# Kernel optimization log

Hardware: AMD Instinct MI355X
Metric: run time of the kernel (lower is better)

## Reference

```python
import math
import jax, jax.numpy as jnp
import numpy as np

D_MODEL = 2048
NUM_EXPERTS = 64
Z_LOSS_COEF = 1e-3
AUX_LOSS_COEF = 1e-2
CAPACITY_FACTOR = 1.0
MIN_CAPACITY = 4


def setup_inputs() -> dict:
    key = jax.random.key(0)
    kx, kw = jax.random.split(key)
    x = jax.random.normal(kx, (4, 4096, D_MODEL), dtype=jnp.float32)
    W = 0.02 * jax.random.normal(kw, (NUM_EXPERTS, D_MODEL), dtype=jnp.float32)  # gate weight [E, D]
    return {"x": x, "W": W}


def reference(x, W):
    B, T, D = x.shape
    N = B * T                      # num_tokens
    E = W.shape[0]
    x_flat = x.reshape(N, D)

    logits = jnp.einsum("nd,ed->ne", x_flat, W)          # gate GEMM [N, E]
    probs = jax.nn.softmax(logits, axis=-1)

    # z-loss: mean(logsumexp(logits)^2)
    z_loss = jnp.mean(jnp.square(jax.nn.logsumexp(logits, axis=-1)))

    expert_index = jnp.argmax(logits, axis=-1)            # [N] int
    expert_prob = jnp.take_along_axis(probs, expert_index[:, None], axis=-1)[:, 0]  # [N]

    counts = jnp.bincount(expert_index, length=E)         # [E] int
    f_i = counts.astype(probs.dtype) / N                  # fraction routed per expert
    p_i = jnp.mean(probs, axis=0)                         # mean router prob per expert
    aux_loss = AUX_LOSS_COEF * E * jnp.sum(f_i * p_i) + Z_LOSS_COEF * z_loss

    capacity = max(MIN_CAPACITY, math.ceil(CAPACITY_FACTOR * N / E))  # static int
    return expert_index, expert_prob, counts, capacity, aux_loss
```

## Files before the change

kernel.cpp:

```cpp
#include <hip/hip_runtime.h>
#include <math.h>

#define D_MODEL 2048
#define NE      64
#define TB      64
#define KHALF   1024
#define KC      64
#define NCH     (KHALF / KC)
#define FB_KC   32
#define FB_NCH  (D_MODEL / FB_KC)

typedef _Float16 half8 __attribute__((ext_vector_type(8)));
typedef float    f32x4 __attribute__((ext_vector_type(4)));

#define CVT1(F, HV, LV, J) do {                                               \
    float _f = (F);                                                           \
    _Float16 _h = (_Float16)_f;                                               \
    HV[J] = _h;                                                               \
    LV[J] = (_Float16)(_f - (float)_h);                                       \
} while (0)

__global__ __launch_bounds__(256) void wcvt_kernel(
    const float* __restrict__ W, short* __restrict__ Wh, short* __restrict__ Wl)
{
    const int e = blockIdx.x, t = threadIdx.x, c = t * 8;
    const float* src = W + (size_t)e * D_MODEL + c;
    float4 v0 = *(const float4*)src;
    float4 v1 = *(const float4*)(src + 4);
    half8 hv, lv;
    CVT1(v0.x * 64.0f, hv, lv, 0); CVT1(v0.y * 64.0f, hv, lv, 1);
    CVT1(v0.z * 64.0f, hv, lv, 2); CVT1(v0.w * 64.0f, hv, lv, 3);
    CVT1(v1.x * 64.0f, hv, lv, 4); CVT1(v1.y * 64.0f, hv, lv, 5);
    CVT1(v1.z * 64.0f, hv, lv, 6); CVT1(v1.w * 64.0f, hv, lv, 7);
    *(half8*)(Wh + (size_t)e * D_MODEL + c) = hv;
    *(half8*)(Wl + (size_t)e * D_MODEL + c) = lv;
}

__global__ __launch_bounds__(512, 2) void router_fused_v3(
    const float* __restrict__ x, const short* __restrict__ Whg,
    const short* __restrict__ Wlg, float* __restrict__ out,
    float* __restrict__ ws_prob, float* __restrict__ ws_z,
    int* __restrict__ ws_cnt, int Ntok)
{
    __shared__ __align__(16) char smem[65536];

    const int t  = threadIdx.x;
    const int b  = blockIdx.x;
    const int m0 = b * TB;
    const int g  = t >> 8;
    const int tg = t & 255;
    const int l  = tg & 63;
    const int wv = tg >> 6;
    const int k0 = g * KHALF;

    char* gbase = smem + g * 32768;

    float (*sL)[NE + 1] = (float (*)[NE + 1])smem;
    float (*red8)[8]    = (float (*)[8])(smem + 16640);
    int   (*arg8)[8]    = (int (*)[8])(smem + 18688);
    float* smax         = (float*)(smem + 20736);
    float* sinv         = (float*)(smem + 20992);
    float (*spart)[NE]  = (float (*)[NE])(smem + 21248);
    int*   hist         = (int*)(smem + 23296);

    const int srow = tg >> 2;
    const int sc   = tg & 3;
    const int ssw  = srow & 7;
    const int sof0 = (srow << 6) + (((sc * 2 + 0) ^ ssw) << 3);
    const int sof1 = (srow << 6) + (((sc * 2 + 1) ^ ssw) << 3);
    const size_t wsrc = (size_t)srow * D_MODEL + k0 + sc * 16;

    const float* abase = x + (size_t)(m0 + wv * 16 + (l & 15)) * D_MODEL
                           + k0 + ((l >> 4) * 8);

    f32x4 acc0 = {0.f,0.f,0.f,0.f}, acc1 = {0.f,0.f,0.f,0.f};
    f32x4 acc2 = {0.f,0.f,0.f,0.f}, acc3 = {0.f,0.f,0.f,0.f};

    uint4  whA0, whA1, wlA0, wlA1;
    uint4  whB0, whB1, wlB0, wlB1;
    float4 aA0, aA1, aA2, aA3;
    float4 aB0, aB1, aB2, aB3;

#define PRE_W(WH0, WH1, WL0, WL1, CH) do {                                    \
    const size_t _o = wsrc + (size_t)(CH) * KC;                               \
    WH0 = *(const uint4*)&Whg[_o];     WH1 = *(const uint4*)&Whg[_o + 8];     \
    WL0 = *(const uint4*)&Wlg[_o];     WL1 = *(const uint4*)&Wlg[_o + 8];     \
} while (0)

#define STORE_W(WH0, WH1, WL0, WL1, BB) do {                                  \
    _Float16* _Wh = (_Float16*)(gbase + (BB) * 16384);                        \
    _Float16* _Wl = (_Float16*)(gbase + (BB) * 16384 + 8192);                 \
    *(uint4*)&_Wh[sof0] = WH0;  *(uint4*)&_Wh[sof1] = WH1;                    \
    *(uint4*)&_Wl[sof0] = WL0;  *(uint4*)&_Wl[sof1] = WL1;                    \
} while (0)

#define PRE_A(PA0, PA1, PA2, PA3, CH) do {                                    \
    const float* _a0 = abase + (size_t)(CH) * KC;                             \
    const float* _a1 = _a0 + 32;                                              \
    PA0 = *(const float4*)_a0; PA1 = *(const float4*)(_a0 + 4);               \
    PA2 = *(const float4*)_a1; PA3 = *(const float4*)(_a1 + 4);               \
} while (0)

#define MFMA_PHASE(BB, PA0, PA1, PA2, PA3) do {                               \
    const _Float16* _Wh = (const _Float16*)(gbase + (BB) * 16384);            \
    const _Float16* _Wl = (const _Float16*)(gbase + (BB) * 16384 + 8192);     \
    const int _rsw = l & 7;                                                   \
    _Pragma("unroll")                                                         \
    for (int kq = 0; kq < 2; ++kq) {                                          \
        half8 _ah, _al;                                                       \
        if (kq == 0) {                                                        \
            CVT1((PA0).x * 8.0f, _ah, _al, 0); CVT1((PA0).y * 8.0f, _ah, _al, 1); \
            CVT1((PA0).z * 8.0f, _ah, _al, 2); CVT1((PA0).w * 8.0f, _ah, _al, 3); \
            CVT1((PA1).x * 8.0f, _ah, _al, 4); CVT1((PA1).y * 8.0f, _ah, _al, 5); \
            CVT1((PA1).z * 8.0f, _ah, _al, 6); CVT1((PA1).w * 8.0f, _ah, _al, 7); \
        } else {                                                              \
            CVT1((PA2).x * 8.0f, _ah, _al, 0); CVT1((PA2).y * 8.0f, _ah, _al, 1); \
            CVT1((PA2).z * 8.0f, _ah, _al, 2); CVT1((PA2).w * 8.0f, _ah, _al, 3); \
            CVT1((PA3).x * 8.0f, _ah, _al, 4); CVT1((PA3).y * 8.0f, _ah, _al, 5); \
            CVT1((PA3).z * 8.0f, _ah, _al, 6); CVT1((PA3).w * 8.0f, _ah, _al, 7); \
        }                                                                     \
        const int _s = kq * 4 + (l >> 4);                                     \
        _Pragma("unroll")                                                     \
        for (int n = 0; n < 4; ++n) {                                         \
            const int _row  = n * 16 + (l & 15);                              \
            const int _woff = (_row << 6) + (((_s ^ (_row & 7))) << 3);       \
            half8 _wh = *(const half8*)&_Wh[_woff];                           \
            half8 _wl = *(const half8*)&_Wl[_woff];                           \
            f32x4 _a = (n == 0) ? acc0 : (n == 1) ? acc1 : (n == 2) ? acc2 : acc3; \
            _a = __builtin_amdgcn_mfma_f32_16x16x32_f16(_al, _wl, _a, 0, 0, 0); \
            _a = __builtin_amdgcn_mfma_f32_16x16x32_f16(_al, _wh, _a, 0, 0, 0); \
            _a = __builtin_amdgcn_mfma_f32_16x16x32_f16(_ah, _wl, _a, 0, 0, 0); \
            _a = __builtin_amdgcn_mfma_f32_16x16x32_f16(_ah, _wh, _a, 0, 0, 0); \
            if (n == 0) acc0 = _a; else if (n == 1) acc1 = _a;                \
            else if (n == 2) acc2 = _a; else acc3 = _a;                       \
        }                                                                     \
    }                                                                         \
} while (0)

    PRE_W(whA0, whA1, wlA0, wlA1, 0);
    STORE_W(whA0, whA1, wlA0, wlA1, 0);
    PRE_W(whB0, whB1, wlB0, wlB1, 1);
    PRE_A(aA0, aA1, aA2, aA3, 0);
    PRE_A(aB0, aB1, aB2, aB3, 1);
    asm volatile("s_waitcnt lgkmcnt(0)" ::: "memory");
    __builtin_amdgcn_s_barrier();

    for (int ch = 0; ch < NCH; ch += 2) {
        if (ch + 1 < NCH) STORE_W(whB0, whB1, wlB0, wlB1, 1);
        if (ch + 2 < NCH) PRE_W(whA0, whA1, wlA0, wlA1, ch + 2);
        MFMA_PHASE(0, aA0, aA1, aA2, aA3);
        if (ch + 2 < NCH) PRE_A(aA0, aA1, aA2, aA3, ch + 2);
        asm volatile("s_waitcnt lgkmcnt(0)" ::: "memory");
        __builtin_amdgcn_s_barrier();
        if (ch + 2 < NCH) STORE_W(whA0, whA1, wlA0, wlA1, 0);
        if (ch + 3 < NCH) PRE_W(whB0, whB1, wlB0, wlB1, ch + 3);
        MFMA_PHASE(1, aB0, aB1, aB2, aB3);
        if (ch + 3 < NCH) PRE_A(aB0, aB1, aB2, aB3, ch + 3);
        asm volatile("s_waitcnt lgkmcnt(0)" ::: "memory");
        __builtin_amdgcn_s_barrier();
    }

    __syncthreads();
    const int rbase = wv * 16 + (l >> 4) * 4;
    const int col0  = l & 15;
    if (g == 1) {
        #pragma unroll
        for (int q = 0; q < 4; ++q) {
            sL[rbase + q][ 0 + col0] = acc0[q];
            sL[rbase + q][16 + col0] = acc1[q];
            sL[rbase + q][32 + col0] = acc2[q];
            sL[rbase + q][48 + col0] = acc3[q];
        }
    }
    __syncthreads();
    if (g == 0) {
        #pragma unroll
        for (int q = 0; q < 4; ++q) {
            sL[rbase + q][ 0 + col0] = (acc0[q] + sL[rbase + q][ 0 + col0]) * (1.0f / 512.0f);
            sL[rbase + q][16 + col0] = (acc1[q] + sL[rbase + q][16 + col0]) * (1.0f / 512.0f);
            sL[rbase + q][32 + col0] = (acc2[q] + sL[rbase + q][32 + col0]) * (1.0f / 512.0f);
            sL[rbase + q][48 + col0] = (acc3[q] + sL[rbase + q][48 + col0]) * (1.0f / 512.0f);
        }
    }
    if (t < NE) hist[t] = 0;
    __syncthreads();

    {
        const int m = t >> 3, qr = t & 7;
        float mx = -3.4e38f; int ag = qr * 8;
        #pragma unroll
        for (int k = 0; k < 8; ++k) {
            const int e = qr * 8 + k;
            float v = sL[m][e];
            if (v > mx) { mx = v; ag = e; }
        }
        red8[m][qr] = mx; arg8[m][qr] = ag;
    }
    __syncthreads();
    if (t < 64) {
        const int m = t;
        float mx = red8[m][0]; int ag = arg8[m][0];
        #pragma unroll
        for (int qr = 1; qr < 8; ++qr)
            if (red8[m][qr] > mx) { mx = red8[m][qr]; ag = arg8[m][qr]; }
        smax[m] = mx;
        out[m0 + m] = (float)ag;
        atomicAdd(&hist[ag], 1);
    }
    __syncthreads();
    {
        const int m = t >> 3, qr = t & 7;
        const float mx = smax[m];
        float s = 0.f;
        #pragma unroll
        for (int k = 0; k < 8; ++k) s += expf(sL[m][qr * 8 + k] - mx);
        red8[m][qr] = s;
    }
    __syncthreads();
    if (t < 64) {
        const int m = t;
        float s = 0.f;
        #pragma unroll
        for (int qr = 0; qr < 8; ++qr) s += red8[m][qr];
        float inv = 1.f / s;
        sinv[m] = inv;
        out[Ntok + m0 + m] = inv;
        float lse = smax[m] + logf(s);
        float z = lse * lse;
        #pragma unroll
        for (int off = 32; off > 0; off >>= 1) z += __shfl_down(z, off, 64);
        if (t == 0) ws_z[b] = z;
    }
    __syncthreads();
    {
        const int e = t & 63, gw = t >> 6;
        float pa = 0.f;
        #pragma unroll
        for (int k = 0; k < 8; ++k) {
            const int m = gw * 8 + k;
            pa += expf(sL[m][e] - smax[m]) * sinv[m];
        }
        spart[gw][e] = pa;
    }
    __syncthreads();
    if (t < NE) {
        float ps = 0.f;
        #pragma unroll
        for (int gw = 0; gw < 8; ++gw) ps += spart[gw][t];
        ws_prob[b * NE + t] = ps;
        ws_cnt[b * NE + t]  = hist[t];
    }
}

__global__ __launch_bounds__(256) void router_final2(
    const float* __restrict__ ws_prob, const float* __restrict__ ws_z,
    const int* __restrict__ ws_cnt, float* __restrict__ out,
    int Ntok, int nblocks)
{
    __shared__ float sp[4][NE];
    __shared__ int   sc[4][NE];
    __shared__ float sz[4];

    const int e = threadIdx.x & 63, g = threadIdx.x >> 6;
    const int per = nblocks / 4;
    const int hi  = (g == 3) ? nblocks : (g + 1) * per;

    float ps = 0.f; int c = 0;
    for (int blk = g * per; blk < hi; ++blk) {
        ps += ws_prob[blk * NE + e];
        c  += ws_cnt[blk * NE + e];
    }
    sp[g][e] = ps; sc[g][e] = c;

    float z = 0.f;
    for (int blk = (int)threadIdx.x; blk < nblocks; blk += 256) z += ws_z[blk];
    #pragma unroll
    for (int off = 32; off > 0; off >>= 1) z += __shfl_down(z, off, 64);
    if (e == 0) sz[g] = z;
    __syncthreads();

    if (threadIdx.x < 64) {
        const int ee = threadIdx.x;
        float pst = ((sp[0][ee] + sp[1][ee]) + sp[2][ee]) + sp[3][ee];
        int   ct  = ((sc[0][ee] + sc[1][ee]) + sc[2][ee]) + sc[3][ee];
        out[2 * Ntok + ee] = (float)ct;

        float fN = (float)Ntok;
        float fp = ((float)ct / fN) * (pst / fN);
        #pragma unroll
        for (int off = 32; off > 0; off >>= 1) fp += __shfl_down(fp, off, 64);
        if (ee == 0) {
            float zt = ((sz[0] + sz[1]) + sz[2]) + sz[3];
            int cap = (Ntok + NE - 1) / NE;
            if (cap < 4) cap = 4;
            float aux = 0.01f * (float)NE * fp + 1e-3f * (zt / fN);
            out[2 * Ntok + NE]     = (float)cap;
            out[2 * Ntok + NE + 1] = aux;
        }
    }
}

__global__ __launch_bounds__(256) void router_main_fb(
    const float* __restrict__ x, const float* __restrict__ W,
    float* __restrict__ out, float* __restrict__ ws_prob,
    float* __restrict__ ws_z, int* __restrict__ ws_cnt, int Ntok)
{
    __shared__ __align__(16) float sX[FB_KC][68];
    __shared__ __align__(16) float sW[FB_KC][68];
    __shared__ float sL[64][65];
    __shared__ float smax[64], sinv[64];
    __shared__ float spart[4][NE];
    __shared__ int   hist[NE];

    const int t = threadIdx.x, b = blockIdx.x, m0 = b * 64;
    const int mq = t & 15, nq = t >> 4;
    const int r1 = t >> 3, r2 = r1 + 32, c1 = (t & 7) << 2;
    const float* xp1 = x + (size_t)(m0 + r1) * D_MODEL + c1;
    const float* xp2 = x + (size_t)(m0 + r2) * D_MODEL + c1;
    const float* wp1 = W + (size_t)r1 * D_MODEL + c1;
    const float* wp2 = W + (size_t)r2 * D_MODEL + c1;
    float4 ax1 = *(const float4*)xp1, ax2 = *(const float4*)xp2;
    float4 aw1 = *(const float4*)wp1, aw2 = *(const float4*)wp2;
    float a1[4][4] = {}, a2[4][4] = {};
    for (int ch = 0; ch < FB_NCH; ++ch) {
        __syncthreads();
        sX[c1+0][r1] = ax1.x; sX[c1+1][r1] = ax1.y; sX[c1+2][r1] = ax1.z; sX[c1+3][r1] = ax1.w;
        sX[c1+0][r2] = ax2.x; sX[c1+1][r2] = ax2.y; sX[c1+2][r2] = ax2.z; sX[c1+3][r2] = ax2.w;
        sW[c1+0][r1] = aw1.x; sW[c1+1][r1] = aw1.y; sW[c1+2][r1] = aw1.z; sW[c1+3][r1] = aw1.w;
        sW[c1+0][r2] = aw2.x; sW[c1+1][r2] = aw2.y; sW[c1+2][r2] = aw2.z; sW[c1+3][r2] = aw2.w;
        __syncthreads();
        if (ch + 1 < FB_NCH) {
            xp1 += FB_KC; xp2 += FB_KC; wp1 += FB_KC; wp2 += FB_KC;
            ax1 = *(const float4*)xp1; ax2 = *(const float4*)xp2;
            aw1 = *(const float4*)wp1; aw2 = *(const float4*)wp2;
        }
        #pragma unroll
        for (int k = 0; k < FB_KC; ++k) {
            float4 xa = *(const float4*)&sX[k][mq << 2];
            float4 wb = *(const float4*)&sW[k][nq << 2];
            float (*A)[4] = (k < FB_KC / 2) ? a1 : a2;
            A[0][0] = fmaf(xa.x, wb.x, A[0][0]); A[0][1] = fmaf(xa.x, wb.y, A[0][1]);
            A[0][2] = fmaf(xa.x, wb.z, A[0][2]); A[0][3] = fmaf(xa.x, wb.w, A[0][3]);
            A[1][0] = fmaf(xa.y, wb.x, A[1][0]); A[1][1] = fmaf(xa.y, wb.y, A[1][1]);
            A[1][2] = fmaf(xa.y, wb.z, A[1][2]); A[1][3] = fmaf(xa.y, wb.w, A[1][3]);
            A[2][0] = fmaf(xa.z, wb.x, A[2][0]); A[2][1] = fmaf(xa.z, wb.y, A[2][1]);
            A[2][2] = fmaf(xa.z, wb.z, A[2][2]); A[2][3] = fmaf(xa.z, wb.w, A[2][3]);
            A[3][0] = fmaf(xa.w, wb.x, A[3][0]); A[3][1] = fmaf(xa.w, wb.y, A[3][1]);
            A[3][2] = fmaf(xa.w, wb.z, A[3][2]); A[3][3] = fmaf(xa.w, wb.w, A[3][3]);
        }
    }
    #pragma unroll
    for (int i = 0; i < 4; ++i)
        #pragma unroll
        for (int j = 0; j < 4; ++j)
            sL[(mq << 2) + i][(nq << 2) + j] = a1[i][j] + a2[i][j];
    if (t < NE) hist[t] = 0;
    __syncthreads();
    if (t < 64) {
        const int m = t;
        float mx = sL[m][0]; int arg = 0;
        for (int e = 1; e < NE; ++e) { float v = sL[m][e]; if (v > mx) { mx = v; arg = e; } }
        float s = 0.f;
        for (int e = 0; e < NE; ++e) s += expf(sL[m][e] - mx);
        float inv = 1.f / s;
        out[m0 + m] = (float)arg; out[Ntok + m0 + m] = inv;
        smax[m] = mx; sinv[m] = inv;
        atomicAdd(&hist[arg], 1);
        float lse = mx + logf(s); float z = lse * lse;
        for (int off = 32; off > 0; off >>= 1) z += __shfl_down(z, off, 64);
        if (t == 0) ws_z[b] = z;
    }
    __syncthreads();
    {
        const int e = t & 63, mg = t >> 6;
        float pa = 0.f;
        for (int m = mg * 16; m < mg * 16 + 16; ++m) pa += expf(sL[m][e] - smax[m]) * sinv[m];
        spart[mg][e] = pa;
    }
    __syncthreads();
    if (t < NE) {
        ws_prob[b * NE + t] = spart[0][t] + spart[1][t] + spart[2][t] + spart[3][t];
        ws_cnt[b * NE + t]  = hist[t];
    }
}

extern "C" void kernel_launch(void* const* d_in, const int* in_sizes, int n_in,
                              void* d_out, int out_size, void* d_ws, size_t ws_size,
                              hipStream_t stream)
{
    const float* x = (const float*)d_in[0];
    const float* W = (const float*)d_in[1];
    float* out = (float*)d_out;

    const int Ntok = in_sizes[0] / D_MODEL;
    const int nblk = Ntok / TB;

    const size_t wh_elems = (size_t)NE * D_MODEL;
    const size_t need = wh_elems * 2 * 2
                      + ((size_t)nblk * NE + nblk) * 4
                      + (size_t)nblk * NE * 4 + 1024;

    if ((Ntok % TB) == 0 && (nblk % 4) == 0 && ws_size >= need) {
        short* wsh     = (short*)d_ws;
        short* wsl     = wsh + wh_elems;
        float* ws_prob = (float*)(wsl + wh_elems);
        float* ws_z    = ws_prob + (size_t)nblk * NE;
        int*   ws_cnt  = (int*)(ws_z + nblk);

        wcvt_kernel<<<NE, 256, 0, stream>>>(W, wsh, wsl);
        router_fused_v3<<<nblk, 512, 0, stream>>>(x, wsh, wsl, out,
                                                  ws_prob, ws_z, ws_cnt, Ntok);
        router_final2<<<1, 256, 0, stream>>>(ws_prob, ws_z, ws_cnt, out, Ntok, nblk);
    } else {
        const int nb = Ntok / 64;
        float* ws_prob = (float*)d_ws;
        float* ws_z    = ws_prob + (size_t)nb * NE;
        int*   ws_cnt  = (int*)(ws_z + nb);
        router_main_fb<<<nb, 256, 0, stream>>>(x, W, out, ws_prob, ws_z, ws_cnt, Ntok);
        router_final2<<<1, 256, 0, stream>>>(ws_prob, ws_z, ws_cnt, out, Ntok, nb);
    }
}
```

Measured before the change: 58.51 us.

## Split K across four thread groups with 1024-thread blocks

The fused router kernel now splits the 2048-wide reduction into four quarters handled by four 256-thread groups in a 1024-thread block, instead of two halves in 512-thread blocks. Partial logits are combined in shared memory through sequential group stores, and the softmax, argmax and z-loss epilogue is re-indexed for 1024 threads. The goal is more parallelism and latency hiding per 64-token tile. In exchange the block needs 128KB of LDS and runs at one block per CU, with extra barriers during the reduction.

```diff
diff --git a/kernel.cpp b/kernel.cpp
--- a/kernel.cpp
+++ b/kernel.cpp
@@ -4,9 +4,9 @@
 #define D_MODEL 2048
 #define NE      64
 #define TB      64
-#define KHALF   1024
+#define KQUAR   512
 #define KC      64
-#define NCH     (KHALF / KC)
+#define NCH     (KQUAR / KC)
 #define FB_KC   32
 #define FB_NCH  (D_MODEL / FB_KC)
 
@@ -36,13 +36,13 @@
     *(half8*)(Wl + (size_t)e * D_MODEL + c) = lv;
 }
 
-__global__ __launch_bounds__(512, 2) void router_fused_v3(
+__global__ __launch_bounds__(1024, 1) void router_fused_v5(
     const float* __restrict__ x, const short* __restrict__ Whg,
     const short* __restrict__ Wlg, float* __restrict__ out,
     float* __restrict__ ws_prob, float* __restrict__ ws_z,
     int* __restrict__ ws_cnt, int Ntok)
 {
-    __shared__ __align__(16) char smem[65536];
+    __shared__ __align__(16) char smem[131072];
 
     const int t  = threadIdx.x;
     const int b  = blockIdx.x;
@@ -51,17 +51,17 @@
     const int tg = t & 255;
     const int l  = tg & 63;
     const int wv = tg >> 6;
-    const int k0 = g * KHALF;
+    const int k0 = g * KQUAR;
 
     char* gbase = smem + g * 32768;
 
-    float (*sL)[NE + 1] = (float (*)[NE + 1])smem;
-    float (*red8)[8]    = (float (*)[8])(smem + 16640);
-    int   (*arg8)[8]    = (int (*)[8])(smem + 18688);
-    float* smax         = (float*)(smem + 20736);
-    float* sinv         = (float*)(smem + 20992);
-    float (*spart)[NE]  = (float (*)[NE])(smem + 21248);
-    int*   hist         = (int*)(smem + 23296);
+    float (*sL)[NE + 1]  = (float (*)[NE + 1])smem;
+    float (*red16)[16]   = (float (*)[16])(smem + 16640);
+    int   (*arg16)[16]   = (int (*)[16])(smem + 20736);
+    float* smax          = (float*)(smem + 24832);
+    float* sinv          = (float*)(smem + 25088);
+    float (*spart)[NE]   = (float (*)[NE])(smem + 25344);
+    int*   hist          = (int*)(smem + 29440);
 
     const int srow = tg >> 2;
     const int sc   = tg & 3;
@@ -104,7 +104,6 @@
 #define MFMA_PHASE(BB, PA0, PA1, PA2, PA3) do {                               \
     const _Float16* _Wh = (const _Float16*)(gbase + (BB) * 16384);            \
     const _Float16* _Wl = (const _Float16*)(gbase + (BB) * 16384 + 8192);     \
-    const int _rsw = l & 7;                                                   \
     _Pragma("unroll")                                                         \
     for (int kq = 0; kq < 2; ++kq) {                                          \
         half8 _ah, _al;                                                       \
@@ -163,7 +162,7 @@
     __syncthreads();
     const int rbase = wv * 16 + (l >> 4) * 4;
     const int col0  = l & 15;
-    if (g == 1) {
+    if (g == 3) {
         #pragma unroll
         for (int q = 0; q < 4; ++q) {
             sL[rbase + q][ 0 + col0] = acc0[q];
@@ -173,6 +172,26 @@
         }
     }
     __syncthreads();
+    if (g == 2) {
+        #pragma unroll
+        for (int q = 0; q < 4; ++q) {
+            sL[rbase + q][ 0 + col0] += acc0[q];
+            sL[rbase + q][16 + col0] += acc1[q];
+            sL[rbase + q][32 + col0] += acc2[q];
+            sL[rbase + q][48 + col0] += acc3[q];
+        }
+    }
+    __syncthreads();
+    if (g == 1) {
+        #pragma unroll
+        for (int q = 0; q < 4; ++q) {
+            sL[rbase + q][ 0 + col0] += acc0[q];
+            sL[rbase + q][16 + col0] += acc1[q];
+            sL[rbase + q][32 + col0] += acc2[q];
+            sL[rbase + q][48 + col0] += acc3[q];
+        }
+    }
+    __syncthreads();
     if (g == 0) {
         #pragma unroll
         for (int q = 0; q < 4; ++q) {
@@ -186,42 +205,42 @@
     __syncthreads();
 
     {
-        const int m = t >> 3, qr = t & 7;
-        float mx = -3.4e38f; int ag = qr * 8;
-        #pragma unroll
-        for (int k = 0; k < 8; ++k) {
-            const int e = qr * 8 + k;
+        const int m = t >> 4, qr = t & 15;
+        float mx = -3.4e38f; int ag = qr * 4;
+        #pragma unroll
+        for (int k = 0; k < 4; ++k) {
+            const int e = qr * 4 + k;
             float v = sL[m][e];
             if (v > mx) { mx = v; ag = e; }
         }
-        red8[m][qr] = mx; arg8[m][qr] = ag;
+        red16[m][qr] = mx; arg16[m][qr] = ag;
     }
     __syncthreads();
     if (t < 64) {
         const int m = t;
-        float mx = red8[m][0]; int ag = arg8[m][0];
-        #pragma unroll
-        for (int qr = 1; qr < 8; ++qr)
-            if (red8[m][qr] > mx) { mx = red8[m][qr]; ag = arg8[m][qr]; }
+        float mx = red16[m][0]; int ag = arg16[m][0];
+        #pragma unroll
+        for (int qr = 1; qr < 16; ++qr)
+            if (red16[m][qr] > mx) { mx = red16[m][qr]; ag = arg16[m][qr]; }
         smax[m] = mx;
         out[m0 + m] = (float)ag;
         atomicAdd(&hist[ag], 1);
     }
     __syncthreads();
     {
-        const int m = t >> 3, qr = t & 7;
+        const int m = t >> 4, qr = t & 15;
         const float mx = smax[m];
         float s = 0.f;
         #pragma unroll
-        for (int k = 0; k < 8; ++k) s += expf(sL[m][qr * 8 + k] - mx);
-        red8[m][qr] = s;
+        for (int k = 0; k < 4; ++k) s += expf(sL[m][qr * 4 + k] - mx);
+        red16[m][qr] = s;
     }
     __syncthreads();
     if (t < 64) {
         const int m = t;
         float s = 0.f;
         #pragma unroll
-        for (int qr = 0; qr < 8; ++qr) s += red8[m][qr];
+        for (int qr = 0; qr < 16; ++qr) s += red16[m][qr];
         float inv = 1.f / s;
         sinv[m] = inv;
         out[Ntok + m0 + m] = inv;
@@ -236,8 +255,8 @@
         const int e = t & 63, gw = t >> 6;
         float pa = 0.f;
         #pragma unroll
-        for (int k = 0; k < 8; ++k) {
-            const int m = gw * 8 + k;
+        for (int k = 0; k < 4; ++k) {
+            const int m = gw * 4 + k;
             pa += expf(sL[m][e] - smax[m]) * sinv[m];
         }
         spart[gw][e] = pa;
@@ -246,7 +265,7 @@
     if (t < NE) {
         float ps = 0.f;
         #pragma unroll
-        for (int gw = 0; gw < 8; ++gw) ps += spart[gw][t];
+        for (int gw = 0; gw < 16; ++gw) ps += spart[gw][t];
         ws_prob[b * NE + t] = ps;
         ws_cnt[b * NE + t]  = hist[t];
     }
@@ -408,8 +427,8 @@
         int*   ws_cnt  = (int*)(ws_z + nblk);
 
         wcvt_kernel<<<NE, 256, 0, stream>>>(W, wsh, wsl);
-        router_fused_v3<<<nblk, 512, 0, stream>>>(x, wsh, wsl, out,
-                                                  ws_prob, ws_z, ws_cnt, Ntok);
+        router_fused_v5<<<nblk, 1024, 0, stream>>>(x, wsh, wsl, out,
+                                                   ws_prob, ws_z, ws_cnt, Ntok);
         router_final2<<<1, 256, 0, stream>>>(ws_prob, ws_z, ws_cnt, out, Ntok, nblk);
     } else {
         const int nb = Ntok / 64;
```

Result: no change. 58.88 us (+0.6%).
